# Kernel optimization log

Measured on AMD Instinct MI355X. Metric: run time of the kernel, lower is better.

The kernel has to match this reference:

```python
import jax, jax.numpy as jnp
import numpy as np

B, S, D, H = 4, 2048, 768, 12
DH = D // H  # 64


def setup_inputs() -> dict:
    key = jax.random.key(0)
    ks = jax.random.split(key, 7)
    return {
        "sequences": jax.random.normal(ks[0], (B, S, D), dtype=jnp.float32),
        "wq": jax.random.normal(ks[1], (H, DH, DH), dtype=jnp.float32) / np.sqrt(DH),
        "bq": jax.random.normal(ks[2], (H, DH), dtype=jnp.float32) * 0.02,
        "wk": jax.random.normal(ks[3], (H, DH, DH), dtype=jnp.float32) / np.sqrt(DH),
        "bk": jax.random.normal(ks[4], (H, DH), dtype=jnp.float32) * 0.02,
        "wv": jax.random.normal(ks[5], (H, DH, DH), dtype=jnp.float32) / np.sqrt(DH),
        "bv": jax.random.normal(ks[6], (H, DH), dtype=jnp.float32) * 0.02,
    }


def reference(sequences, wq, bq, wk, bk, wv, bv):
    # split channels into heads: [B, S, H, DH]
    xh = sequences.reshape(B, S, H, DH)
    # per-head linear projections (weight applied as x @ W^T + b, matching nn.Linear)
    q = jnp.einsum("bshd,hed->bshe", xh, wq) + bq  # [B,S,H,DH]
    k = jnp.einsum("bshd,hed->bshe", xh, wk) + bk
    v = jnp.einsum("bshd,hed->bshe", xh, wv) + bv
    scale = 1.0 / np.sqrt(DH).astype(np.float32)
    scores = jnp.einsum("bqhd,bkhd->bhqk", q, k) * scale  # [B,H,S,S]
    attn = jax.nn.softmax(scores, axis=-1)
    out = jnp.einsum("bhqk,bkhd->bqhd", attn, v)  # [B,S,H,DH]
    return out.reshape(B, S, D)
```

## Files before the change

kernel.cpp:

```cpp
#include <hip/hip_runtime.h>

#define NB 4
#define NS 2048
#define ND 768
#define NH 12
#define NDH 64
#define NT (NS / 128)
#define XPITCH 72
#define SSCALE 0.18033688011112043f

typedef __bf16 bf16x8 __attribute__((ext_vector_type(8)));
typedef float  f32x4  __attribute__((ext_vector_type(4)));
typedef unsigned int u32;

#define MFMA16(a, b, c) __builtin_amdgcn_mfma_f32_16x16x32_bf16(a, b, c, 0, 0, 0)

__device__ __forceinline__ u32 packbf(float a, float b) {
    u32 ua = __builtin_bit_cast(u32, a) + 0x8000u;
    u32 ub = __builtin_bit_cast(u32, b) + 0x8000u;
    return __builtin_amdgcn_perm(ub, ua, 0x07060302u);
}

__device__ __forceinline__ bf16x8 cvt8(float4 a, float4 b) {
    union { u32 u[4]; bf16x8 v; } r;
    r.u[0] = packbf(a.x, a.y); r.u[1] = packbf(a.z, a.w);
    r.u[2] = packbf(b.x, b.y); r.u[3] = packbf(b.z, b.w);
    return r.v;
}

__device__ __forceinline__ __bf16 f2bf(float f) {
    u32 u = __builtin_bit_cast(u32, f) + 0x8000u;
    unsigned short s = (unsigned short)(u >> 16);
    return __builtin_bit_cast(__bf16, s);
}

__device__ __forceinline__ void gl16(const __bf16* g, __bf16* l) {
    __builtin_amdgcn_global_load_lds(
        (const __attribute__((address_space(1))) unsigned int*)g,
        (__attribute__((address_space(3))) unsigned int*)l,
        16, 0, 0);
}


__global__ __launch_bounds__(256, 4) void proj_kernel(
    const float* __restrict__ x,
    const float* __restrict__ wq, const float* __restrict__ bq,
    const float* __restrict__ wk, const float* __restrict__ bk,
    const float* __restrict__ wv, const float* __restrict__ bv,
    __bf16* __restrict__ qws, __bf16* __restrict__ kws, __bf16* __restrict__ vtws)
{
    const int st = blockIdx.x, h = blockIdx.y, b = blockIdx.z;
    const int s0 = st * 64;
    const int tid = threadIdx.x;

    __shared__ __align__(16) __bf16 Xs[64 * XPITCH];
    __shared__ __align__(16) __bf16 Tv[64 * XPITCH];

    const int r = tid >> 2, f = tid & 3;
    const int lane = tid & 63, w = tid >> 6, col = lane & 15, quad = lane >> 4;

    const size_t wrow = (size_t)(h * NDH + w * 16 + col) * NDH;
    const float* wq0 = wq + wrow + quad * 8;
    const float* wk0 = wk + wrow + quad * 8;
    const float* wv0 = wv + wrow + quad * 8;
    const bf16x8 wqa0 = cvt8(*(const float4*)(wq0),      *(const float4*)(wq0 + 4));
    const bf16x8 wqa1 = cvt8(*(const float4*)(wq0 + 32), *(const float4*)(wq0 + 36));
    const bf16x8 wka0 = cvt8(*(const float4*)(wk0),      *(const float4*)(wk0 + 4));
    const bf16x8 wka1 = cvt8(*(const float4*)(wk0 + 32), *(const float4*)(wk0 + 36));
    const bf16x8 wva0 = cvt8(*(const float4*)(wv0),      *(const float4*)(wv0 + 4));
    const bf16x8 wva1 = cvt8(*(const float4*)(wv0 + 32), *(const float4*)(wv0 + 36));

    float bqs[4], bks[4], bvs[4];
#pragma unroll
    for (int rr = 0; rr < 4; ++rr) {
        const int e = h * NDH + w * 16 + quad * 4 + rr;
        bqs[rr] = bq[e] * SSCALE;
        bks[rr] = bk[e];
        bvs[rr] = bv[e];
    }

    const size_t bh = (size_t)(b * NH + h);

    {
        const float* xrow = x + (size_t)(b * NS + s0 + r) * ND + h * NDH + f * 16;
        const float4 v0 = *(const float4*)(xrow);
        const float4 v1 = *(const float4*)(xrow + 4);
        const float4 v2 = *(const float4*)(xrow + 8);
        const float4 v3 = *(const float4*)(xrow + 12);
        *(bf16x8*)&Xs[r * XPITCH + f * 16]     = cvt8(v0, v1);
        *(bf16x8*)&Xs[r * XPITCH + f * 16 + 8] = cvt8(v2, v3);
    }
    __syncthreads();

    const int e0 = w * 16 + quad * 4;
    const int jj = e0 >> 5;
    const int qa = (e0 >> 3) & 3;
    const int hf = (e0 >> 2) & 1;
    const int Lf = qa * 16 + col;
    const int kt = st >> 1;

#pragma unroll
    for (int nt = 0; nt < 4; ++nt) {
        const bf16x8 xb0 = *(const bf16x8*)&Xs[(nt * 16 + col) * XPITCH + quad * 8];
        const bf16x8 xb1 = *(const bf16x8*)&Xs[(nt * 16 + col) * XPITCH + 32 + quad * 8];
        f32x4 aq = {0.f, 0.f, 0.f, 0.f};
        f32x4 ak = {0.f, 0.f, 0.f, 0.f};
        f32x4 av = {0.f, 0.f, 0.f, 0.f};
        aq = MFMA16(wqa0, xb0, aq); aq = MFMA16(wqa1, xb1, aq);
        ak = MFMA16(wka0, xb0, ak); ak = MFMA16(wka1, xb1, ak);
        av = MFMA16(wva0, xb0, av); av = MFMA16(wva1, xb1, av);

        union { u32 u[2]; uint2 v; } pq, pk;
        pq.u[0] = packbf(fmaf(aq[0], SSCALE, bqs[0]), fmaf(aq[1], SSCALE, bqs[1]));
        pq.u[1] = packbf(fmaf(aq[2], SSCALE, bqs[2]), fmaf(aq[3], SSCALE, bqs[3]));
        pk.u[0] = packbf(ak[0] + bks[0], ak[1] + bks[1]);
        pk.u[1] = packbf(ak[2] + bks[2], ak[3] + bks[3]);

        const int wa = (st & 1) * 2 + (nt >> 1);
        const int mt = nt & 1;
        const size_t kidx = ((((((size_t)bh * 16 + kt) * 4 + wa) * 2 + mt) * 2 + jj) * 64 + Lf) * 8 + hf * 4;
        const size_t qidx = (((((size_t)bh * 32 + st) * 4 + nt) * 2 + jj) * 64 + Lf) * 8 + hf * 4;
        *(uint2*)(kws + kidx) = pk.v;
        *(uint2*)(qws + qidx) = pq.v;

        const int pos = ((nt >> 1) << 5) + ((col >> 2) << 3) + ((nt & 1) << 2) + (col & 3);
#pragma unroll
        for (int rr = 0; rr < 4; ++rr)
            Tv[(w * 16 + quad * 4 + rr) * XPITCH + pos] = f2bf(av[rr] + bvs[rr]);
    }
    __syncthreads();

    {
        const uint4 v0 = *(const uint4*)&Tv[r * XPITCH + f * 16];
        const uint4 v1 = *(const uint4*)&Tv[r * XPITCH + f * 16 + 8];
        const int wv_ = (st & 1) * 2 + (f >> 1);
        const int dtv = r >> 4;
        const int colv = r & 15;
        const int L0 = ((f & 1) * 2 + 0) * 16 + colv;
        const int L1 = ((f & 1) * 2 + 1) * 16 + colv;
        const size_t vbase = (((size_t)bh * 16 + kt) * 4 + wv_) * 4 + dtv;
        *(uint4*)(vtws + (vbase * 64 + L0) * 8) = v0;
        *(uint4*)(vtws + (vbase * 64 + L1) * 8) = v1;
    }
}

__global__ __launch_bounds__(256, 3) void attn_kernel(
    const __bf16* __restrict__ qws, const __bf16* __restrict__ kws,
    const __bf16* __restrict__ vtws, float* __restrict__ out)
{
    const int bid = blockIdx.x;
    const int xcd = bid & 7;
    const int j   = bid >> 3;
    const int g   = xcd * 6 + (j >> 5);
    const int qt  = j & 31;
    const int h   = g % NH;
    const int b   = g / NH;

    const int q0 = qt * 64;
    const int tid = threadIdx.x;

    __shared__ __align__(16) unsigned char smem[36864];
    __bf16* ldsK = (__bf16*)smem;
    __bf16* ldsV = (__bf16*)(smem + 16384);
    float* slabA = (float*)smem;
    float* slabB = (float*)(smem + 17408);
    float* lbuf  = (float*)(smem + 34816);

    const size_t bh = (size_t)(b * NH + h);
    const int lane = tid & 63, w = tid >> 6, col = lane & 15, quad = lane >> 4;

    bf16x8 qb0[4], qb1[4];
    {
        const __bf16* qp = qws + (size_t)bh * 131072 + (size_t)qt * 4096 + lane * 8;
#pragma unroll
        for (int nt = 0; nt < 4; ++nt) {
            qb0[nt] = *(const bf16x8*)(qp + nt * 1024);
            qb1[nt] = *(const bf16x8*)(qp + nt * 1024 + 512);
        }
    }

    const __bf16* kg = kws  + (size_t)bh * 131072 + w * 2048 + lane * 8;
    const __bf16* vg = vtws + (size_t)bh * 131072 + w * 2048 + lane * 8;
    __bf16* lk  = ldsK + w * 2048;
    __bf16* lv  = ldsV + w * 2048;
    const __bf16* lkr = lk + lane * 8;
    const __bf16* lvr = lv + lane * 8;

    float l[4] = {0.f, 0.f, 0.f, 0.f};
    f32x4 o[4][4];
#pragma unroll
    for (int dt = 0; dt < 4; ++dt)
#pragma unroll
        for (int nt = 0; nt < 4; ++nt) o[dt][nt] = (f32x4){0.f, 0.f, 0.f, 0.f};

#pragma unroll
    for (int i = 0; i < 4; ++i) gl16(kg + i * 512, lk + i * 512);
#pragma unroll
    for (int i = 0; i < 4; ++i) gl16(vg + i * 512, lv + i * 512);

    for (int kt = 0; kt < NT; ++kt) {
        asm volatile("s_waitcnt vmcnt(0)" ::: "memory");
        __builtin_amdgcn_sched_barrier(0);

        bf16x8 ka[2][2], va[4];
        ka[0][0] = *(const bf16x8*)(lkr);
        ka[0][1] = *(const bf16x8*)(lkr + 512);
        ka[1][0] = *(const bf16x8*)(lkr + 1024);
        ka[1][1] = *(const bf16x8*)(lkr + 1536);
        va[0] = *(const bf16x8*)(lvr);
        va[1] = *(const bf16x8*)(lvr + 512);
        va[2] = *(const bf16x8*)(lvr + 1024);
        va[3] = *(const bf16x8*)(lvr + 1536);

        asm volatile("s_waitcnt lgkmcnt(0)" ::: "memory");
        __builtin_amdgcn_sched_barrier(0);

        if (kt + 1 < NT) {
            const __bf16* kgn = kg + (size_t)(kt + 1) * 8192;
            const __bf16* vgn = vg + (size_t)(kt + 1) * 8192;
#pragma unroll
            for (int i = 0; i < 4; ++i) gl16(kgn + i * 512, lk + i * 512);
#pragma unroll
            for (int i = 0; i < 4; ++i) gl16(vgn + i * 512, lv + i * 512);
        }

#pragma unroll
        for (int nt = 0; nt < 4; ++nt) {
            f32x4 sA = {0.f, 0.f, 0.f, 0.f};
            f32x4 sB = {0.f, 0.f, 0.f, 0.f};
            sA = MFMA16(ka[0][0], qb0[nt], sA); sA = MFMA16(ka[0][1], qb1[nt], sA);
            sB = MFMA16(ka[1][0], qb0[nt], sB); sB = MFMA16(ka[1][1], qb1[nt], sB);

            const float p0 = __builtin_amdgcn_exp2f(sA[0]);
            const float p1 = __builtin_amdgcn_exp2f(sA[1]);
            const float p2 = __builtin_amdgcn_exp2f(sA[2]);
            const float p3 = __builtin_amdgcn_exp2f(sA[3]);
            const float p4 = __builtin_amdgcn_exp2f(sB[0]);
            const float p5 = __builtin_amdgcn_exp2f(sB[1]);
            const float p6 = __builtin_amdgcn_exp2f(sB[2]);
            const float p7 = __builtin_amdgcn_exp2f(sB[3]);
            l[nt] += ((p0 + p1) + (p2 + p3)) + ((p4 + p5) + (p6 + p7));

            union { u32 u[4]; bf16x8 v; } pb;
            pb.u[0] = packbf(p0, p1);
            pb.u[1] = packbf(p2, p3);
            pb.u[2] = packbf(p4, p5);
            pb.u[3] = packbf(p6, p7);

#pragma unroll
            for (int dt = 0; dt < 4; ++dt)
                o[dt][nt] = MFMA16(va[dt], pb.v, o[dt][nt]);
        }
    }

#pragma unroll
    for (int nt = 0; nt < 4; ++nt) {
        l[nt] += __shfl_xor(l[nt], 16, 64);
        l[nt] += __shfl_xor(l[nt], 32, 64);
    }

    __syncthreads();
    if (quad == 0) {
#pragma unroll
        for (int nt = 0; nt < 4; ++nt)
            lbuf[w * 64 + nt * 16 + col] = l[nt];
    }
    __syncthreads();

    float scale[4];
#pragma unroll
    for (int nt = 0; nt < 4; ++nt) {
        const int qi = nt * 16 + col;
        const float Lt = (lbuf[qi] + lbuf[64 + qi]) + (lbuf[128 + qi] + lbuf[192 + qi]);
        scale[nt] = 1.0f / Lt;
    }
    __syncthreads();
#pragma unroll
    for (int dt = 0; dt < 4; ++dt)
#pragma unroll
        for (int nt = 0; nt < 4; ++nt) o[dt][nt] *= scale[nt];

    if (w == 0 || w == 2) {
        float* s = (w == 0) ? slabA : slabB;
#pragma unroll
        for (int dt = 0; dt < 4; ++dt)
#pragma unroll
            for (int nt = 0; nt < 4; ++nt)
                *(f32x4*)&s[(nt * 16 + col) * 68 + dt * 16 + quad * 4] = o[dt][nt];
    }
    __syncthreads();
    if (w == 1 || w == 3) {
        float* s = (w == 1) ? slabA : slabB;
#pragma unroll
        for (int dt = 0; dt < 4; ++dt)
#pragma unroll
            for (int nt = 0; nt < 4; ++nt) {
                f32x4* p = (f32x4*)&s[(nt * 16 + col) * 68 + dt * 16 + quad * 4];
                *p = *p + o[dt][nt];
            }
    }
    __syncthreads();

    const int qr = tid >> 2, fq = tid & 3;
#pragma unroll
    for (int j2 = 0; j2 < 4; ++j2) {
        const f32x4 a = *(const f32x4*)&slabA[qr * 68 + fq * 16 + j2 * 4];
        const f32x4 c = *(const f32x4*)&slabB[qr * 68 + fq * 16 + j2 * 4];
        *(f32x4*)&out[(size_t)(b * NS + q0 + qr) * ND + h * NDH + fq * 16 + j2 * 4] = a + c;
    }
}

extern "C" void kernel_launch(void* const* d_in, const int* in_sizes, int n_in,
                              void* d_out, int out_size, void* d_ws, size_t ws_size,
                              hipStream_t stream) {
    (void)in_sizes; (void)n_in; (void)out_size; (void)ws_size;
    const float* x  = (const float*)d_in[0];
    const float* wq = (const float*)d_in[1];
    const float* bq = (const float*)d_in[2];
    const float* wk = (const float*)d_in[3];
    const float* bk = (const float*)d_in[4];
    const float* wv = (const float*)d_in[5];
    const float* bv = (const float*)d_in[6];
    float* out = (float*)d_out;

    __bf16* qws  = (__bf16*)d_ws;
    __bf16* kws  = qws + (size_t)NB * NH * NS * NDH;
    __bf16* vtws = kws + (size_t)NB * NH * NS * NDH;

    dim3 grid(NS / 64, NH, NB);
    proj_kernel<<<grid, 256, 0, stream>>>(x, wq, bq, wk, bk, wv, bv, qws, kws, vtws);
    attn_kernel<<<dim3(NS / 64 * NH * NB), 256, 0, stream>>>(qws, kws, vtws, out);
}
```

Baseline: 168.4 us.

## Split attention waves 2x2 over query and key halves instead of four key slices

Reassigns the four waves of each attention block into a 2x2 grid: each wave now holds 32 query rows and walks half of the keys in 64-key steps, 32 iterations, where before every wave held all 64 queries and a quarter-slice of each 128-key tile. This halves the per-wave accumulator and Q registers and shrinks the cross-wave reduction to a single slab, so LDS drops and launch bounds rise to 4 blocks per SIMD for more occupancy. In exchange each wave loads twice as many K/V tiles, with more loop iterations and waitcnt stalls per unit of MFMA work.

```diff
diff --git a/kernel.cpp b/kernel.cpp
--- a/kernel.cpp
+++ b/kernel.cpp
@@ -5,7 +5,6 @@
 #define ND 768
 #define NH 12
 #define NDH 64
-#define NT (NS / 128)
 #define XPITCH 72
 #define SSCALE 0.18033688011112043f
 
@@ -144,7 +143,7 @@
     }
 }
 
-__global__ __launch_bounds__(256, 3) void attn_kernel(
+__global__ __launch_bounds__(256, 4) void attn_kernel(
     const __bf16* __restrict__ qws, const __bf16* __restrict__ kws,
     const __bf16* __restrict__ vtws, float* __restrict__ out)
 {
@@ -159,46 +158,47 @@
     const int q0 = qt * 64;
     const int tid = threadIdx.x;
 
-    __shared__ __align__(16) unsigned char smem[36864];
+    __shared__ __align__(16) unsigned char smem[33280];
     __bf16* ldsK = (__bf16*)smem;
     __bf16* ldsV = (__bf16*)(smem + 16384);
-    float* slabA = (float*)smem;
-    float* slabB = (float*)(smem + 17408);
-    float* lbuf  = (float*)(smem + 34816);
+    float* slab  = (float*)smem;
+    float* lbuf  = (float*)(smem + 32768);
 
     const size_t bh = (size_t)(b * NH + h);
     const int lane = tid & 63, w = tid >> 6, col = lane & 15, quad = lane >> 4;
-
-    bf16x8 qb0[4], qb1[4];
+    const int wq = w >> 1, wk = w & 1;
+
+    bf16x8 qb0[2], qb1[2];
     {
-        const __bf16* qp = qws + (size_t)bh * 131072 + (size_t)qt * 4096 + lane * 8;
-#pragma unroll
-        for (int nt = 0; nt < 4; ++nt) {
+        const __bf16* qp = qws + (size_t)bh * 131072 + (size_t)qt * 4096
+                         + wq * 2048 + lane * 8;
+#pragma unroll
+        for (int nt = 0; nt < 2; ++nt) {
             qb0[nt] = *(const bf16x8*)(qp + nt * 1024);
             qb1[nt] = *(const bf16x8*)(qp + nt * 1024 + 512);
         }
     }
 
-    const __bf16* kg = kws  + (size_t)bh * 131072 + w * 2048 + lane * 8;
-    const __bf16* vg = vtws + (size_t)bh * 131072 + w * 2048 + lane * 8;
+    const __bf16* kg = kws  + (size_t)bh * 131072 + wk * 2048 + lane * 8;
+    const __bf16* vg = vtws + (size_t)bh * 131072 + wk * 2048 + lane * 8;
     __bf16* lk  = ldsK + w * 2048;
     __bf16* lv  = ldsV + w * 2048;
     const __bf16* lkr = lk + lane * 8;
     const __bf16* lvr = lv + lane * 8;
 
-    float l[4] = {0.f, 0.f, 0.f, 0.f};
-    f32x4 o[4][4];
+    float l[2] = {0.f, 0.f};
+    f32x4 o[4][2];
 #pragma unroll
     for (int dt = 0; dt < 4; ++dt)
 #pragma unroll
-        for (int nt = 0; nt < 4; ++nt) o[dt][nt] = (f32x4){0.f, 0.f, 0.f, 0.f};
+        for (int nt = 0; nt < 2; ++nt) o[dt][nt] = (f32x4){0.f, 0.f, 0.f, 0.f};
 
 #pragma unroll
     for (int i = 0; i < 4; ++i) gl16(kg + i * 512, lk + i * 512);
 #pragma unroll
     for (int i = 0; i < 4; ++i) gl16(vg + i * 512, lv + i * 512);
 
-    for (int kt = 0; kt < NT; ++kt) {
+    for (int kt = 0; kt < 32; ++kt) {
         asm volatile("s_waitcnt vmcnt(0)" ::: "memory");
         __builtin_amdgcn_sched_barrier(0);
 
@@ -215,9 +215,9 @@
         asm volatile("s_waitcnt lgkmcnt(0)" ::: "memory");
         __builtin_amdgcn_sched_barrier(0);
 
-        if (kt + 1 < NT) {
-            const __bf16* kgn = kg + (size_t)(kt + 1) * 8192;
-            const __bf16* vgn = vg + (size_t)(kt + 1) * 8192;
+        if (kt + 1 < 32) {
+            const __bf16* kgn = kg + (size_t)(kt + 1) * 4096;
+            const __bf16* vgn = vg + (size_t)(kt + 1) * 4096;
 #pragma unroll
             for (int i = 0; i < 4; ++i) gl16(kgn + i * 512, lk + i * 512);
 #pragma unroll
@@ -225,7 +225,7 @@
         }
 
 #pragma unroll
-        for (int nt = 0; nt < 4; ++nt) {
+        for (int nt = 0; nt < 2; ++nt) {
             f32x4 sA = {0.f, 0.f, 0.f, 0.f};
             f32x4 sB = {0.f, 0.f, 0.f, 0.f};
             sA = MFMA16(ka[0][0], qb0[nt], sA); sA = MFMA16(ka[0][1], qb1[nt], sA);
@@ -254,7 +254,7 @@
     }
 
 #pragma unroll
-    for (int nt = 0; nt < 4; ++nt) {
+    for (int nt = 0; nt < 2; ++nt) {
         l[nt] += __shfl_xor(l[nt], 16, 64);
         l[nt] += __shfl_xor(l[nt], 32, 64);
     }
@@ -262,40 +262,36 @@
     __syncthreads();
     if (quad == 0) {
 #pragma unroll
-        for (int nt = 0; nt < 4; ++nt)
-            lbuf[w * 64 + nt * 16 + col] = l[nt];
-    }
-    __syncthreads();
-
-    float scale[4];
-#pragma unroll
-    for (int nt = 0; nt < 4; ++nt) {
-        const int qi = nt * 16 + col;
-        const float Lt = (lbuf[qi] + lbuf[64 + qi]) + (lbuf[128 + qi] + lbuf[192 + qi]);
-        scale[nt] = 1.0f / Lt;
-    }
-    __syncthreads();
+        for (int nt = 0; nt < 2; ++nt)
+            lbuf[wk * 64 + wq * 32 + nt * 16 + col] = l[nt];
+    }
+    __syncthreads();
+
+    float scale[2];
+#pragma unroll
+    for (int nt = 0; nt < 2; ++nt) {
+        const int ri = wq * 32 + nt * 16 + col;
+        scale[nt] = 1.0f / (lbuf[ri] + lbuf[64 + ri]);
+    }
 #pragma unroll
     for (int dt = 0; dt < 4; ++dt)
 #pragma unroll
-        for (int nt = 0; nt < 4; ++nt) o[dt][nt] *= scale[nt];
-
-    if (w == 0 || w == 2) {
-        float* s = (w == 0) ? slabA : slabB;
+        for (int nt = 0; nt < 2; ++nt) o[dt][nt] *= scale[nt];
+
+    if (wk == 0) {
 #pragma unroll
         for (int dt = 0; dt < 4; ++dt)
 #pragma unroll
-            for (int nt = 0; nt < 4; ++nt)
-                *(f32x4*)&s[(nt * 16 + col) * 68 + dt * 16 + quad * 4] = o[dt][nt];
-    }
-    __syncthreads();
-    if (w == 1 || w == 3) {
-        float* s = (w == 1) ? slabA : slabB;
+            for (int nt = 0; nt < 2; ++nt)
+                *(f32x4*)&slab[(wq * 32 + nt * 16 + col) * 68 + dt * 16 + quad * 4] = o[dt][nt];
+    }
+    __syncthreads();
+    if (wk == 1) {
 #pragma unroll
         for (int dt = 0; dt < 4; ++dt)
 #pragma unroll
-            for (int nt = 0; nt < 4; ++nt) {
-                f32x4* p = (f32x4*)&s[(nt * 16 + col) * 68 + dt * 16 + quad * 4];
+            for (int nt = 0; nt < 2; ++nt) {
+                f32x4* p = (f32x4*)&slab[(wq * 32 + nt * 16 + col) * 68 + dt * 16 + quad * 4];
                 *p = *p + o[dt][nt];
             }
     }
@@ -304,9 +300,8 @@
     const int qr = tid >> 2, fq = tid & 3;
 #pragma unroll
     for (int j2 = 0; j2 < 4; ++j2) {
-        const f32x4 a = *(const f32x4*)&slabA[qr * 68 + fq * 16 + j2 * 4];
-        const f32x4 c = *(const f32x4*)&slabB[qr * 68 + fq * 16 + j2 * 4];
-        *(f32x4*)&out[(size_t)(b * NS + q0 + qr) * ND + h * NDH + fq * 16 + j2 * 4] = a + c;
+        const f32x4 a = *(const f32x4*)&slab[qr * 68 + fq * 16 + j2 * 4];
+        *(f32x4*)&out[(size_t)(b * NS + q0 + qr) * ND + h * NDH + fq * 16 + j2 * 4] = a;
     }
 }
 
```

Result: no change. 171.1 us (+1.6%).
